# Performance work log

Hardware: AMD Instinct MI355X
Metric: run time of the kernel (lower is better)

Reference implementation:

```python
import jax, jax.numpy as jnp
import numpy as np

EPS = 1e-5
GROUPS = 8

def _bn(x, g, b, axes):
    # training-mode batch norm over `axes`, channel axis = 1
    m = jnp.mean(x, axis=axes, keepdims=True)
    v = jnp.var(x, axis=axes, keepdims=True)
    shp = (1, -1) + (1,) * (x.ndim - 2)
    return (x - m) / jnp.sqrt(v + EPS) * g.reshape(shp) + b.reshape(shp)

def setup_inputs() -> dict:
    key = jax.random.key(0)
    k0, k1, k2 = jax.random.split(key, 3)
    N, C, T, V = 64, 256, 64, 25
    out_planes = 256
    gp = out_planes // GROUPS  # 32
    x = jax.random.normal(k0, (N, C, T, V), jnp.float32)
    w_qkv = jax.random.normal(k1, (2 * out_planes, C), jnp.float32) * np.float32(np.sqrt(1.0 / C))
    relative = jax.random.normal(k2, (2 * gp, 2 * V - 1), jnp.float32) * np.float32(np.sqrt(1.0 / gp))
    return {
        "x": x,
        "w_qkv": w_qkv,
        "relative": relative,
        "bn_qkv_g": jnp.ones(2 * out_planes, jnp.float32),
        "bn_qkv_b": jnp.zeros(2 * out_planes, jnp.float32),
        "bn_sim_g": jnp.ones(3 * GROUPS, jnp.float32),
        "bn_sim_b": jnp.zeros(3 * GROUPS, jnp.float32),
        "bn_out_g": jnp.ones(2 * out_planes, jnp.float32),
        "bn_out_b": jnp.zeros(2 * out_planes, jnp.float32),
    }

def reference(x, w_qkv, relative, bn_qkv_g, bn_qkv_b, bn_sim_g, bn_sim_b, bn_out_g, bn_out_b):
    N, C, T, V = x.shape
    out_planes = w_qkv.shape[0] // 2
    gp = out_planes // GROUPS
    K = V  # kernel_size == V by construction
    # static relative index table
    qi = np.arange(K)[None, :]
    ki = np.arange(K)[:, None]
    flat_idx = (ki - qi + K - 1).reshape(-1)
    # mean over frames T (permute(0,2,1,3) then mean over dim1 == mean over axis 2)
    y = jnp.mean(x, axis=2)  # [N, C, V]
    # 1x1 conv qkv + BN1d
    qkv = _bn(jnp.einsum('oc,ncv->nov', w_qkv, y), bn_qkv_g, bn_qkv_b, (0, 2))
    qkv = qkv.reshape(N, GROUPS, 2 * gp, V)
    q, k, v = qkv[:, :, : gp // 2], qkv[:, :, gp // 2: gp], qkv[:, :, gp:]
    all_emb = relative[:, flat_idx].reshape(2 * gp, K, K)
    q_e, k_e, v_e = all_emb[: gp // 2], all_emb[gp // 2: gp], all_emb[gp:]
    qr = jnp.einsum('ngci,cij->ngij', q, q_e)
    kr = jnp.einsum('ngci,cij->ngij', k, k_e).swapaxes(2, 3)
    qk = jnp.einsum('ngci,ngcj->ngij', q, k)
    stacked = jnp.concatenate([qk, qr, kr], axis=1)  # [N, 3*groups, V, V]
    stacked = _bn(stacked, bn_sim_g, bn_sim_b, (0, 2, 3)).reshape(N, 3, GROUPS, V, V).sum(axis=1)
    sim = jax.nn.softmax(stacked, axis=3)  # [N, groups, V, V]
    sv = jnp.einsum('ngij,ngcj->ngci', sim, v)
    sve = jnp.einsum('ngij,cij->ngci', sim, v_e)
    so = jnp.concatenate([sv, sve], axis=-1).reshape(N, 2 * out_planes, V)
    o = _bn(so, bn_out_g, bn_out_b, (0, 2)).reshape(N, out_planes, 2, V).sum(axis=2)
    o = jax.nn.sigmoid(o)[:, :, None, :]  # [N, out_planes, 1, V]
    return x + x * o
```

## Files before the change

### kernel.cpp

```cpp
#include <hip/hip_runtime.h>
#include <cmath>

#define NN 64
#define CC 256
#define TT 64
#define VV 25
#define OO 512
#define GG 8
#define NV (NN*VV)
#define STK 625

__global__ __launch_bounds__(256) void k_mean(const float* __restrict__ x,
                                              float* __restrict__ y) {
    __shared__ float tile[TT * VV];
    int b = blockIdx.x;
    const float4* x4 = (const float4*)(x + (size_t)b * (TT * VV));
    float4* t4 = (float4*)tile;
    for (int i = threadIdx.x; i < (TT * VV) / 4; i += 256) t4[i] = x4[i];
    __syncthreads();
    if (threadIdx.x < VV) {
        float s = 0.f;
        #pragma unroll
        for (int t = 0; t < TT; ++t) s += tile[t * VV + threadIdx.x];
        y[(size_t)b * VV + threadIdx.x] = s * (1.0f / TT);
    }
}

__global__ __launch_bounds__(256) void k_gemm(const float* __restrict__ y,
                                              const float* __restrict__ w,
                                              float* __restrict__ qkv) {
    __shared__ float ys[CC][VV + 1];
    int n = blockIdx.x >> 3, oc = blockIdx.x & 7;
    const float* yp = y + (size_t)n * CC * VV;
    for (int i = threadIdx.x; i < CC * VV; i += 256) ys[i / VV][i % VV] = yp[i];
    __syncthreads();
    int t = threadIdx.x;
    if (t >= 200) return;
    int v = t % VV, o0 = t / VV;
    int obase = oc * 64 + o0;
    float acc[8] = {0, 0, 0, 0, 0, 0, 0, 0};
    for (int c = 0; c < CC; c += 4) {
        float y0 = ys[c][v], y1 = ys[c + 1][v], y2 = ys[c + 2][v], y3 = ys[c + 3][v];
        #pragma unroll
        for (int u = 0; u < 8; ++u) {
            const float4 w4 = *(const float4*)&w[(size_t)(obase + u * 8) * CC + c];
            acc[u] += y0 * w4.x + y1 * w4.y + y2 * w4.z + y3 * w4.w;
        }
    }
    #pragma unroll
    for (int u = 0; u < 8; ++u)
        qkv[((size_t)n * OO + obase + u * 8) * VV + v] = acc[u];
}

__global__ __launch_bounds__(256) void k_stats_nv(const float* __restrict__ t,
                                                  const float* __restrict__ g,
                                                  const float* __restrict__ b,
                                                  float* __restrict__ scale,
                                                  float* __restrict__ shift) {
    int ch = blockIdx.x;
    float s = 0.f, s2 = 0.f;
    for (int i = threadIdx.x; i < NV; i += 256) {
        int n = i / VV, v = i - n * VV;
        float val = t[((size_t)n * OO + ch) * VV + v];
        s += val; s2 += val * val;
    }
    __shared__ float ra[256], rb[256];
    ra[threadIdx.x] = s; rb[threadIdx.x] = s2;
    __syncthreads();
    for (int off = 128; off > 0; off >>= 1) {
        if (threadIdx.x < off) {
            ra[threadIdx.x] += ra[threadIdx.x + off];
            rb[threadIdx.x] += rb[threadIdx.x + off];
        }
        __syncthreads();
    }
    if (threadIdx.x == 0) {
        float m = ra[0] * (1.0f / NV);
        float var = rb[0] * (1.0f / NV) - m * m;
        float sc = g[ch] * rsqrtf(var + 1e-5f);
        scale[ch] = sc;
        shift[ch] = b[ch] - m * sc;
    }
}

__global__ __launch_bounds__(256) void k_scores(const float* __restrict__ qkv,
                                                const float* __restrict__ rel,
                                                const float* __restrict__ qsc,
                                                const float* __restrict__ qsh,
                                                float* __restrict__ stk) {
    int n = blockIdx.x >> 3, gidx = blockIdx.x & 7;
    __shared__ float qs[16][VV], ks[16][VV], rs[32][49];
    int t = threadIdx.x;
    for (int i = t; i < 32 * VV; i += 256) {
        int c = i / VV, v = i - c * VV;
        int o = gidx * 64 + c;
        float val = qkv[((size_t)n * OO + o) * VV + v] * qsc[o] + qsh[o];
        if (c < 16) qs[c][v] = val; else ks[c - 16][v] = val;
    }
    for (int i = t; i < 32 * 49; i += 256) rs[i / 49][i % 49] = rel[i];
    __syncthreads();
    for (int ij = t; ij < STK; ij += 256) {
        int i = ij / VV, j = ij - (ij / VV) * VV;
        float aqk = 0.f, aqr = 0.f, akr = 0.f;
        #pragma unroll
        for (int c = 0; c < 16; ++c) {
            float qv = qs[c][i], kv = ks[c][j];
            aqk += qv * kv;
            aqr += qv * rs[c][i - j + 24];
            akr += kv * rs[16 + c][j - i + 24];
        }
        size_t base = (size_t)n * 24;
        stk[(base + gidx) * STK + ij]      = aqk;
        stk[(base + 8 + gidx) * STK + ij]  = aqr;
        stk[(base + 16 + gidx) * STK + ij] = akr;
    }
}

__global__ __launch_bounds__(256) void k_stats24_a(const float* __restrict__ stk,
                                                   float* __restrict__ part) {
    int ch = blockIdx.x >> 4, chunk = blockIdx.x & 15;
    float s = 0.f, s2 = 0.f;
    for (int i = threadIdx.x; i < 4 * STK; i += 256) {
        int n = chunk * 4 + i / STK, r = i - (i / STK) * STK;
        float v = stk[((size_t)n * 24 + ch) * STK + r];
        s += v; s2 += v * v;
    }
    __shared__ float ra[256], rb[256];
    ra[threadIdx.x] = s; rb[threadIdx.x] = s2;
    __syncthreads();
    for (int off = 128; off > 0; off >>= 1) {
        if (threadIdx.x < off) {
            ra[threadIdx.x] += ra[threadIdx.x + off];
            rb[threadIdx.x] += rb[threadIdx.x + off];
        }
        __syncthreads();
    }
    if (threadIdx.x == 0) {
        part[(ch * 16 + chunk) * 2]     = ra[0];
        part[(ch * 16 + chunk) * 2 + 1] = rb[0];
    }
}

__global__ __launch_bounds__(64) void k_stats24_b(const float* __restrict__ part,
                                                  const float* __restrict__ g,
                                                  const float* __restrict__ b,
                                                  float* __restrict__ scale,
                                                  float* __restrict__ shift) {
    int ch = threadIdx.x;
    if (ch < 24) {
        float s = 0.f, s2 = 0.f;
        for (int k = 0; k < 16; ++k) {
            s  += part[(ch * 16 + k) * 2];
            s2 += part[(ch * 16 + k) * 2 + 1];
        }
        float m = s * (1.0f / 40000.0f);
        float var = s2 * (1.0f / 40000.0f) - m * m;
        float sc = g[ch] * rsqrtf(var + 1e-5f);
        scale[ch] = sc;
        shift[ch] = b[ch] - m * sc;
    }
}

__global__ __launch_bounds__(256) void k_attnout(const float* __restrict__ stk,
                                                 const float* __restrict__ qkv,
                                                 const float* __restrict__ rel,
                                                 const float* __restrict__ qsc,
                                                 const float* __restrict__ qsh,
                                                 const float* __restrict__ ssc,
                                                 const float* __restrict__ ssh,
                                                 float* __restrict__ so) {
    int n = blockIdx.x >> 3, gidx = blockIdx.x & 7;
    __shared__ float S[STK];
    __shared__ float vs[32][VV];
    __shared__ float rs[32][49];
    int t = threadIdx.x;
    const size_t sb = (size_t)n * 24 * STK;
    float sc0 = ssc[gidx],      sh0 = ssh[gidx];
    float sc1 = ssc[8 + gidx],  sh1 = ssh[8 + gidx];
    float sc2 = ssc[16 + gidx], sh2 = ssh[16 + gidx];
    for (int ij = t; ij < STK; ij += 256) {
        float a = stk[sb + (size_t)gidx * STK + ij] * sc0 + sh0;
        a += stk[sb + (size_t)(8 + gidx) * STK + ij] * sc1 + sh1;
        a += stk[sb + (size_t)(16 + gidx) * STK + ij] * sc2 + sh2;
        S[ij] = a;
    }
    for (int i = t; i < 32 * VV; i += 256) {
        int c = i / VV, v = i - (i / VV) * VV;
        int o = gidx * 64 + 32 + c;
        vs[c][v] = qkv[((size_t)n * OO + o) * VV + v] * qsc[o] + qsh[o];
    }
    for (int i = t; i < 32 * 49; i += 256) rs[i / 49][i % 49] = rel[32 * 49 + i];
    __syncthreads();
    if (t < VV) {
        int i = t;
        float m = -1e30f;
        #pragma unroll
        for (int j = 0; j < VV; ++j) m = fmaxf(m, S[i * VV + j]);
        float sum = 0.f;
        float e[VV];
        #pragma unroll
        for (int j = 0; j < VV; ++j) { e[j] = expf(S[i * VV + j] - m); sum += e[j]; }
        float inv = 1.0f / sum;
        #pragma unroll
        for (int j = 0; j < VV; ++j) S[i * VV + j] = e[j] * inv;
    }
    __syncthreads();
    for (int idx = t; idx < 32 * VV; idx += 256) {
        int c = idx / VV, i = idx - (idx / VV) * VV;
        float sv = 0.f, sve = 0.f;
        #pragma unroll
        for (int j = 0; j < VV; ++j) {
            float p = S[i * VV + j];
            sv  += p * vs[c][j];
            sve += p * rs[c][i - j + 24];
        }
        size_t o = (size_t)(gidx * 32 + c) * 2;
        so[((size_t)n * OO + o) * VV + i]     = sv;
        so[((size_t)n * OO + o + 1) * VV + i] = sve;
    }
}

__global__ __launch_bounds__(256) void k_final(const float* __restrict__ x,
                                               const float* __restrict__ so,
                                               const float* __restrict__ osc,
                                               const float* __restrict__ osh,
                                               float* __restrict__ out) {
    int b = blockIdx.x;
    int n = b >> 8, p = b & 255;
    __shared__ float orow[VV];
    if (threadIdx.x < VV) {
        int v = threadIdx.x;
        int o0 = 2 * p, o1 = 2 * p + 1;
        float a  = so[((size_t)n * OO + o0) * VV + v] * osc[o0] + osh[o0];
        float c2 = so[((size_t)n * OO + o1) * VV + v] * osc[o1] + osh[o1];
        float z = a + c2;
        orow[v] = 1.0f + 1.0f / (1.0f + expf(-z));
    }
    __syncthreads();
    const float4* x4 = (const float4*)(x + (size_t)b * (TT * VV));
    float4* y4 = (float4*)(out + (size_t)b * (TT * VV));
    for (int wv = threadIdx.x; wv < (TT * VV) / 4; wv += 256) {
        float4 xv = x4[wv];
        int e = 4 * wv;
        int v0 = e % VV;
        float4 r;
        int v;
        v = v0;                      r.x = xv.x * orow[v];
        v = v0 + 1; if (v >= VV) v -= VV; r.y = xv.y * orow[v];
        v = v0 + 2; if (v >= VV) v -= VV; r.z = xv.z * orow[v];
        v = v0 + 3; if (v >= VV) v -= VV; r.w = xv.w * orow[v];
        y4[wv] = r;
    }
}

extern "C" void kernel_launch(void* const* d_in, const int* in_sizes, int n_in,
                              void* d_out, int out_size, void* d_ws, size_t ws_size,
                              hipStream_t stream) {
    (void)in_sizes; (void)n_in; (void)out_size; (void)ws_size;
    const float* x        = (const float*)d_in[0];
    const float* w_qkv    = (const float*)d_in[1];
    const float* relative = (const float*)d_in[2];
    const float* bn_qkv_g = (const float*)d_in[3];
    const float* bn_qkv_b = (const float*)d_in[4];
    const float* bn_sim_g = (const float*)d_in[5];
    const float* bn_sim_b = (const float*)d_in[6];
    const float* bn_out_g = (const float*)d_in[7];
    const float* bn_out_b = (const float*)d_in[8];
    float* out = (float*)d_out;

    float* ws = (float*)d_ws;
    float* w_y    = ws;
    float* w_qkvp = ws + 409600;
    float* w_stk  = ws + 1228800;
    float* w_so   = ws + 2188800;
    float* qsc    = ws + 3008000;
    float* qsh    = qsc + 512;
    float* ssc    = qsh + 512;
    float* ssh    = ssc + 24;
    float* osc    = ssh + 24;
    float* osh    = osc + 512;
    float* w_part = osh + 512;

    k_mean<<<NN * CC, 256, 0, stream>>>(x, w_y);
    k_gemm<<<NN * 8, 256, 0, stream>>>(w_y, w_qkv, w_qkvp);
    k_stats_nv<<<OO, 256, 0, stream>>>(w_qkvp, bn_qkv_g, bn_qkv_b, qsc, qsh);
    k_scores<<<NN * GG, 256, 0, stream>>>(w_qkvp, relative, qsc, qsh, w_stk);
    k_stats24_a<<<24 * 16, 256, 0, stream>>>(w_stk, w_part);
    k_stats24_b<<<1, 64, 0, stream>>>(w_part, bn_sim_g, bn_sim_b, ssc, ssh);
    k_attnout<<<NN * GG, 256, 0, stream>>>(w_stk, w_qkvp, relative, qsc, qsh, ssc, ssh, w_so);
    k_stats_nv<<<OO, 256, 0, stream>>>(w_so, bn_out_g, bn_out_b, osc, osh);
    k_final<<<NN * CC, 256, 0, stream>>>(x, w_so, osc, osh, out);
}
```

Before: 281.4 us.

## Fuse middle stages into one cooperative kernel with grid syncs and atomic BN stats

New measurement: 364.2 us. 29.4% more time.

```diff
diff --git a/kernel.cpp b/kernel.cpp
--- a/kernel.cpp
+++ b/kernel.cpp
@@ -1,4 +1,5 @@
 #include <hip/hip_runtime.h>
+#include <hip/hip_cooperative_groups.h>
 #include <cmath>
 
 #define NN 64
@@ -10,10 +11,16 @@
 #define NV (NN*VV)
 #define STK 625
 
+namespace cg = cooperative_groups;
+
 __global__ __launch_bounds__(256) void k_mean(const float* __restrict__ x,
-                                              float* __restrict__ y) {
+                                              float* __restrict__ y,
+                                              float* __restrict__ accz) {
     __shared__ float tile[TT * VV];
     int b = blockIdx.x;
+    if (b == 0) {
+        for (int i = threadIdx.x; i < 2096; i += 256) accz[i] = 0.f;
+    }
     const float4* x4 = (const float4*)(x + (size_t)b * (TT * VV));
     float4* t4 = (float4*)tile;
     for (int i = threadIdx.x; i < (TT * VV) / 4; i += 256) t4[i] = x4[i];
@@ -26,213 +33,202 @@
     }
 }
 
-__global__ __launch_bounds__(256) void k_gemm(const float* __restrict__ y,
-                                              const float* __restrict__ w,
-                                              float* __restrict__ qkv) {
-    __shared__ float ys[CC][VV + 1];
-    int n = blockIdx.x >> 3, oc = blockIdx.x & 7;
-    const float* yp = y + (size_t)n * CC * VV;
-    for (int i = threadIdx.x; i < CC * VV; i += 256) ys[i / VV][i % VV] = yp[i];
-    __syncthreads();
-    int t = threadIdx.x;
-    if (t >= 200) return;
-    int v = t % VV, o0 = t / VV;
-    int obase = oc * 64 + o0;
-    float acc[8] = {0, 0, 0, 0, 0, 0, 0, 0};
-    for (int c = 0; c < CC; c += 4) {
-        float y0 = ys[c][v], y1 = ys[c + 1][v], y2 = ys[c + 2][v], y3 = ys[c + 3][v];
+__global__ __launch_bounds__(256, 2) void k_mid(const float* __restrict__ y,
+                                                const float* __restrict__ w,
+                                                const float* __restrict__ rel,
+                                                const float* __restrict__ gq,
+                                                const float* __restrict__ bq,
+                                                const float* __restrict__ gs,
+                                                const float* __restrict__ bs,
+                                                float* __restrict__ qacc,
+                                                float* __restrict__ sacc,
+                                                float* __restrict__ oacc,
+                                                float* __restrict__ so) {
+    cg::grid_group grid = cg::this_grid();
+
+    __shared__ __align__(16) float ys[CC * (VV + 1)];
+    __shared__ float qs[64 * (VV + 1)];
+    __shared__ float S3[3 * STK];
+    __shared__ float P[STK];
+    __shared__ float rs[32 * 49];
+    __shared__ float csc[64], csh[64];
+    __shared__ float simp[6];
+    __shared__ float sred[24];
+
+    const int tid = threadIdx.x;
+    const int nb = blockIdx.x >> 3, gb = blockIdx.x & 7;
+
+    {
+        const float* yp = y + (size_t)nb * (CC * VV);
+        for (int i = tid; i < CC * VV; i += 256) {
+            int c = i / VV, v = i - c * VV;
+            ys[c * (VV + 1) + v] = yp[i];
+        }
+        __syncthreads();
+        if (tid < 200) {
+            int v = tid % VV, o0 = tid / VV;
+            const float* wp = w + (size_t)(gb * 64 + o0) * CC;
+            float acc[8] = {0, 0, 0, 0, 0, 0, 0, 0};
+            for (int c = 0; c < CC; c += 4) {
+                float y0 = ys[c * (VV + 1) + v],       y1 = ys[(c + 1) * (VV + 1) + v];
+                float y2 = ys[(c + 2) * (VV + 1) + v], y3 = ys[(c + 3) * (VV + 1) + v];
+                #pragma unroll
+                for (int u = 0; u < 8; ++u) {
+                    const float4 w4 = *(const float4*)(wp + (size_t)u * 8 * CC + c);
+                    acc[u] += y0 * w4.x + y1 * w4.y + y2 * w4.z + y3 * w4.w;
+                }
+            }
+            #pragma unroll
+            for (int u = 0; u < 8; ++u) qs[(o0 + u * 8) * (VV + 1) + v] = acc[u];
+        }
+        __syncthreads();
+        if (tid < 64) {
+            float s = 0.f, s2 = 0.f;
+            #pragma unroll
+            for (int v = 0; v < VV; ++v) {
+                float val = qs[tid * (VV + 1) + v];
+                s += val; s2 += val * val;
+            }
+            atomicAdd(&qacc[gb * 64 + tid], s);
+            atomicAdd(&qacc[512 + gb * 64 + tid], s2);
+        }
+    }
+    grid.sync();
+
+    {
+        if (tid < 64) {
+            int ch = gb * 64 + tid;
+            float m = qacc[ch] * (1.0f / NV);
+            float var = qacc[512 + ch] * (1.0f / NV) - m * m;
+            float sc = gq[ch] * rsqrtf(var + 1e-5f);
+            csc[tid] = sc;
+            csh[tid] = bq[ch] - m * sc;
+        }
+        __syncthreads();
+        for (int i = tid; i < 64 * VV; i += 256) {
+            int c = i / VV, v = i - c * VV;
+            qs[c * (VV + 1) + v] = qs[c * (VV + 1) + v] * csc[c] + csh[c];
+        }
+        for (int i = tid; i < 32 * 49; i += 256) rs[i] = rel[i];
+        __syncthreads();
+        float ls0 = 0.f, ls1 = 0.f, ls2 = 0.f, ls3 = 0.f, ls4 = 0.f, ls5 = 0.f;
+        for (int ij = tid; ij < STK; ij += 256) {
+            int i = ij / VV, j = ij - (ij / VV) * VV;
+            float aqk = 0.f, aqr = 0.f, akr = 0.f;
+            #pragma unroll
+            for (int c = 0; c < 16; ++c) {
+                float qv = qs[c * (VV + 1) + i], kv = qs[(16 + c) * (VV + 1) + j];
+                aqk += qv * kv;
+                aqr += qv * rs[c * 49 + i - j + 24];
+                akr += kv * rs[(16 + c) * 49 + j - i + 24];
+            }
+            S3[ij] = aqk; S3[STK + ij] = aqr; S3[2 * STK + ij] = akr;
+            ls0 += aqk; ls1 += aqk * aqk;
+            ls2 += aqr; ls3 += aqr * aqr;
+            ls4 += akr; ls5 += akr * akr;
+        }
         #pragma unroll
-        for (int u = 0; u < 8; ++u) {
-            const float4 w4 = *(const float4*)&w[(size_t)(obase + u * 8) * CC + c];
-            acc[u] += y0 * w4.x + y1 * w4.y + y2 * w4.z + y3 * w4.w;
-        }
-    }
-    #pragma unroll
-    for (int u = 0; u < 8; ++u)
-        qkv[((size_t)n * OO + obase + u * 8) * VV + v] = acc[u];
-}
-
-__global__ __launch_bounds__(256) void k_stats_nv(const float* __restrict__ t,
-                                                  const float* __restrict__ g,
-                                                  const float* __restrict__ b,
-                                                  float* __restrict__ scale,
-                                                  float* __restrict__ shift) {
-    int ch = blockIdx.x;
-    float s = 0.f, s2 = 0.f;
-    for (int i = threadIdx.x; i < NV; i += 256) {
-        int n = i / VV, v = i - n * VV;
-        float val = t[((size_t)n * OO + ch) * VV + v];
-        s += val; s2 += val * val;
-    }
-    __shared__ float ra[256], rb[256];
-    ra[threadIdx.x] = s; rb[threadIdx.x] = s2;
-    __syncthreads();
-    for (int off = 128; off > 0; off >>= 1) {
-        if (threadIdx.x < off) {
-            ra[threadIdx.x] += ra[threadIdx.x + off];
-            rb[threadIdx.x] += rb[threadIdx.x + off];
-        }
-        __syncthreads();
-    }
-    if (threadIdx.x == 0) {
-        float m = ra[0] * (1.0f / NV);
-        float var = rb[0] * (1.0f / NV) - m * m;
-        float sc = g[ch] * rsqrtf(var + 1e-5f);
-        scale[ch] = sc;
-        shift[ch] = b[ch] - m * sc;
-    }
-}
-
-__global__ __launch_bounds__(256) void k_scores(const float* __restrict__ qkv,
-                                                const float* __restrict__ rel,
-                                                const float* __restrict__ qsc,
-                                                const float* __restrict__ qsh,
-                                                float* __restrict__ stk) {
-    int n = blockIdx.x >> 3, gidx = blockIdx.x & 7;
-    __shared__ float qs[16][VV], ks[16][VV], rs[32][49];
-    int t = threadIdx.x;
-    for (int i = t; i < 32 * VV; i += 256) {
-        int c = i / VV, v = i - c * VV;
-        int o = gidx * 64 + c;
-        float val = qkv[((size_t)n * OO + o) * VV + v] * qsc[o] + qsh[o];
-        if (c < 16) qs[c][v] = val; else ks[c - 16][v] = val;
-    }
-    for (int i = t; i < 32 * 49; i += 256) rs[i / 49][i % 49] = rel[i];
-    __syncthreads();
-    for (int ij = t; ij < STK; ij += 256) {
-        int i = ij / VV, j = ij - (ij / VV) * VV;
-        float aqk = 0.f, aqr = 0.f, akr = 0.f;
-        #pragma unroll
-        for (int c = 0; c < 16; ++c) {
-            float qv = qs[c][i], kv = ks[c][j];
-            aqk += qv * kv;
-            aqr += qv * rs[c][i - j + 24];
-            akr += kv * rs[16 + c][j - i + 24];
-        }
-        size_t base = (size_t)n * 24;
-        stk[(base + gidx) * STK + ij]      = aqk;
-        stk[(base + 8 + gidx) * STK + ij]  = aqr;
-        stk[(base + 16 + gidx) * STK + ij] = akr;
-    }
-}
-
-__global__ __launch_bounds__(256) void k_stats24_a(const float* __restrict__ stk,
-                                                   float* __restrict__ part) {
-    int ch = blockIdx.x >> 4, chunk = blockIdx.x & 15;
-    float s = 0.f, s2 = 0.f;
-    for (int i = threadIdx.x; i < 4 * STK; i += 256) {
-        int n = chunk * 4 + i / STK, r = i - (i / STK) * STK;
-        float v = stk[((size_t)n * 24 + ch) * STK + r];
-        s += v; s2 += v * v;
-    }
-    __shared__ float ra[256], rb[256];
-    ra[threadIdx.x] = s; rb[threadIdx.x] = s2;
-    __syncthreads();
-    for (int off = 128; off > 0; off >>= 1) {
-        if (threadIdx.x < off) {
-            ra[threadIdx.x] += ra[threadIdx.x + off];
-            rb[threadIdx.x] += rb[threadIdx.x + off];
-        }
-        __syncthreads();
-    }
-    if (threadIdx.x == 0) {
-        part[(ch * 16 + chunk) * 2]     = ra[0];
-        part[(ch * 16 + chunk) * 2 + 1] = rb[0];
-    }
-}
-
-__global__ __launch_bounds__(64) void k_stats24_b(const float* __restrict__ part,
-                                                  const float* __restrict__ g,
-                                                  const float* __restrict__ b,
-                                                  float* __restrict__ scale,
-                                                  float* __restrict__ shift) {
-    int ch = threadIdx.x;
-    if (ch < 24) {
-        float s = 0.f, s2 = 0.f;
-        for (int k = 0; k < 16; ++k) {
-            s  += part[(ch * 16 + k) * 2];
-            s2 += part[(ch * 16 + k) * 2 + 1];
-        }
-        float m = s * (1.0f / 40000.0f);
-        float var = s2 * (1.0f / 40000.0f) - m * m;
-        float sc = g[ch] * rsqrtf(var + 1e-5f);
-        scale[ch] = sc;
-        shift[ch] = b[ch] - m * sc;
-    }
-}
-
-__global__ __launch_bounds__(256) void k_attnout(const float* __restrict__ stk,
-                                                 const float* __restrict__ qkv,
-                                                 const float* __restrict__ rel,
-                                                 const float* __restrict__ qsc,
-                                                 const float* __restrict__ qsh,
-                                                 const float* __restrict__ ssc,
-                                                 const float* __restrict__ ssh,
-                                                 float* __restrict__ so) {
-    int n = blockIdx.x >> 3, gidx = blockIdx.x & 7;
-    __shared__ float S[STK];
-    __shared__ float vs[32][VV];
-    __shared__ float rs[32][49];
-    int t = threadIdx.x;
-    const size_t sb = (size_t)n * 24 * STK;
-    float sc0 = ssc[gidx],      sh0 = ssh[gidx];
-    float sc1 = ssc[8 + gidx],  sh1 = ssh[8 + gidx];
-    float sc2 = ssc[16 + gidx], sh2 = ssh[16 + gidx];
-    for (int ij = t; ij < STK; ij += 256) {
-        float a = stk[sb + (size_t)gidx * STK + ij] * sc0 + sh0;
-        a += stk[sb + (size_t)(8 + gidx) * STK + ij] * sc1 + sh1;
-        a += stk[sb + (size_t)(16 + gidx) * STK + ij] * sc2 + sh2;
-        S[ij] = a;
-    }
-    for (int i = t; i < 32 * VV; i += 256) {
-        int c = i / VV, v = i - (i / VV) * VV;
-        int o = gidx * 64 + 32 + c;
-        vs[c][v] = qkv[((size_t)n * OO + o) * VV + v] * qsc[o] + qsh[o];
-    }
-    for (int i = t; i < 32 * 49; i += 256) rs[i / 49][i % 49] = rel[32 * 49 + i];
-    __syncthreads();
-    if (t < VV) {
-        int i = t;
-        float m = -1e30f;
-        #pragma unroll
-        for (int j = 0; j < VV; ++j) m = fmaxf(m, S[i * VV + j]);
-        float sum = 0.f;
-        float e[VV];
-        #pragma unroll
-        for (int j = 0; j < VV; ++j) { e[j] = expf(S[i * VV + j] - m); sum += e[j]; }
-        float inv = 1.0f / sum;
-        #pragma unroll
-        for (int j = 0; j < VV; ++j) S[i * VV + j] = e[j] * inv;
-    }
-    __syncthreads();
-    for (int idx = t; idx < 32 * VV; idx += 256) {
-        int c = idx / VV, i = idx - (idx / VV) * VV;
-        float sv = 0.f, sve = 0.f;
-        #pragma unroll
-        for (int j = 0; j < VV; ++j) {
-            float p = S[i * VV + j];
-            sv  += p * vs[c][j];
-            sve += p * rs[c][i - j + 24];
-        }
-        size_t o = (size_t)(gidx * 32 + c) * 2;
-        so[((size_t)n * OO + o) * VV + i]     = sv;
-        so[((size_t)n * OO + o + 1) * VV + i] = sve;
+        for (int off = 32; off > 0; off >>= 1) {
+            ls0 += __shfl_down(ls0, off); ls1 += __shfl_down(ls1, off);
+            ls2 += __shfl_down(ls2, off); ls3 += __shfl_down(ls3, off);
+            ls4 += __shfl_down(ls4, off); ls5 += __shfl_down(ls5, off);
+        }
+        int lane = tid & 63, wid = tid >> 6;
+        if (lane == 0) {
+            sred[wid * 6 + 0] = ls0; sred[wid * 6 + 1] = ls1;
+            sred[wid * 6 + 2] = ls2; sred[wid * 6 + 3] = ls3;
+            sred[wid * 6 + 4] = ls4; sred[wid * 6 + 5] = ls5;
+        }
+        __syncthreads();
+        if (tid < 6) {
+            float t2 = sred[tid] + sred[6 + tid] + sred[12 + tid] + sred[18 + tid];
+            int ch = (tid >> 1) * 8 + gb;
+            atomicAdd(&sacc[(tid & 1) * 24 + ch], t2);
+        }
+    }
+    grid.sync();
+
+    {
+        if (tid < 3) {
+            int ch = tid * 8 + gb;
+            float m = sacc[ch] * (1.0f / 40000.0f);
+            float var = sacc[24 + ch] * (1.0f / 40000.0f) - m * m;
+            float sc = gs[ch] * rsqrtf(var + 1e-5f);
+            simp[tid * 2] = sc;
+            simp[tid * 2 + 1] = bs[ch] - m * sc;
+        }
+        __syncthreads();
+        for (int ij = tid; ij < STK; ij += 256)
+            P[ij] = S3[ij] * simp[0] + simp[1]
+                  + S3[STK + ij] * simp[2] + simp[3]
+                  + S3[2 * STK + ij] * simp[4] + simp[5];
+        for (int i = tid; i < 32 * 49; i += 256) rs[i] = rel[32 * 49 + i];
+        __syncthreads();
+        if (tid < VV) {
+            const int i = tid;
+            float mx = -1e30f;
+            #pragma unroll
+            for (int j = 0; j < VV; ++j) mx = fmaxf(mx, P[i * VV + j]);
+            float e[VV]; float sum = 0.f;
+            #pragma unroll
+            for (int j = 0; j < VV; ++j) { e[j] = expf(P[i * VV + j] - mx); sum += e[j]; }
+            float inv = 1.0f / sum;
+            #pragma unroll
+            for (int j = 0; j < VV; ++j) P[i * VV + j] = e[j] * inv;
+        }
+        __syncthreads();
+        float* svs  = ys;
+        float* sves = ys + 800;
+        for (int idx = tid; idx < 800; idx += 256) {
+            int c = idx / VV, i = idx - (idx / VV) * VV;
+            float sv = 0.f, sve = 0.f;
+            #pragma unroll
+            for (int j = 0; j < VV; ++j) {
+                float p = P[i * VV + j];
+                sv  += p * qs[(32 + c) * (VV + 1) + j];
+                sve += p * rs[c * 49 + i - j + 24];
+            }
+            svs[idx] = sv; sves[idx] = sve;
+        }
+        __syncthreads();
+        if (tid < 64) {
+            int c = tid >> 1;
+            const float* src = (tid & 1) ? (sves + c * VV) : (svs + c * VV);
+            float s = 0.f, s2 = 0.f;
+            #pragma unroll
+            for (int i = 0; i < VV; ++i) { float val = src[i]; s += val; s2 += val * val; }
+            atomicAdd(&oacc[gb * 64 + tid], s);
+            atomicAdd(&oacc[512 + gb * 64 + tid], s2);
+        }
+        float* sop = so + ((size_t)nb * OO + gb * 64) * VV;
+        for (int idx = tid; idx < 1600; idx += 256) {
+            int oc = idx / VV, i = idx - (idx / VV) * VV;
+            int c = oc >> 1;
+            sop[idx] = (oc & 1) ? sves[c * VV + i] : svs[c * VV + i];
+        }
     }
 }
 
 __global__ __launch_bounds__(256) void k_final(const float* __restrict__ x,
                                                const float* __restrict__ so,
-                                               const float* __restrict__ osc,
-                                               const float* __restrict__ osh,
+                                               const float* __restrict__ oacc,
+                                               const float* __restrict__ go,
+                                               const float* __restrict__ bo,
                                                float* __restrict__ out) {
     int b = blockIdx.x;
     int n = b >> 8, p = b & 255;
     __shared__ float orow[VV];
     if (threadIdx.x < VV) {
+        int o0 = 2 * p, o1 = 2 * p + 1;
+        float m0 = oacc[o0] * (1.0f / NV);
+        float var0 = oacc[512 + o0] * (1.0f / NV) - m0 * m0;
+        float sc0 = go[o0] * rsqrtf(var0 + 1e-5f), sh0 = bo[o0] - m0 * sc0;
+        float m1 = oacc[o1] * (1.0f / NV);
+        float var1 = oacc[512 + o1] * (1.0f / NV) - m1 * m1;
+        float sc1 = go[o1] * rsqrtf(var1 + 1e-5f), sh1 = bo[o1] - m1 * sc1;
         int v = threadIdx.x;
-        int o0 = 2 * p, o1 = 2 * p + 1;
-        float a  = so[((size_t)n * OO + o0) * VV + v] * osc[o0] + osh[o0];
-        float c2 = so[((size_t)n * OO + o1) * VV + v] * osc[o1] + osh[o1];
+        float a  = so[((size_t)n * OO + o0) * VV + v] * sc0 + sh0;
+        float c2 = so[((size_t)n * OO + o1) * VV + v] * sc1 + sh1;
         float z = a + c2;
         orow[v] = 1.0f + 1.0f / (1.0f + expf(-z));
     }
@@ -269,25 +265,19 @@
     float* out = (float*)d_out;
 
     float* ws = (float*)d_ws;
-    float* w_y    = ws;
-    float* w_qkvp = ws + 409600;
-    float* w_stk  = ws + 1228800;
-    float* w_so   = ws + 2188800;
-    float* qsc    = ws + 3008000;
-    float* qsh    = qsc + 512;
-    float* ssc    = qsh + 512;
-    float* ssh    = ssc + 24;
-    float* osc    = ssh + 24;
-    float* osh    = osc + 512;
-    float* w_part = osh + 512;
-
-    k_mean<<<NN * CC, 256, 0, stream>>>(x, w_y);
-    k_gemm<<<NN * 8, 256, 0, stream>>>(w_y, w_qkv, w_qkvp);
-    k_stats_nv<<<OO, 256, 0, stream>>>(w_qkvp, bn_qkv_g, bn_qkv_b, qsc, qsh);
-    k_scores<<<NN * GG, 256, 0, stream>>>(w_qkvp, relative, qsc, qsh, w_stk);
-    k_stats24_a<<<24 * 16, 256, 0, stream>>>(w_stk, w_part);
-    k_stats24_b<<<1, 64, 0, stream>>>(w_part, bn_sim_g, bn_sim_b, ssc, ssh);
-    k_attnout<<<NN * GG, 256, 0, stream>>>(w_stk, w_qkvp, relative, qsc, qsh, ssc, ssh, w_so);
-    k_stats_nv<<<OO, 256, 0, stream>>>(w_so, bn_out_g, bn_out_b, osc, osh);
-    k_final<<<NN * CC, 256, 0, stream>>>(x, w_so, osc, osh, out);
-}
+    float* w_y  = ws;
+    float* w_so = ws + 409600;
+    float* qacc = ws + 1228800;
+    float* sacc = qacc + 1024;
+    float* oacc = sacc + 48;
+
+    k_mean<<<NN * CC, 256, 0, stream>>>(x, w_y, qacc);
+
+    void* args[] = {(void*)&w_y, (void*)&w_qkv, (void*)&relative,
+                    (void*)&bn_qkv_g, (void*)&bn_qkv_b,
+                    (void*)&bn_sim_g, (void*)&bn_sim_b,
+                    (void*)&qacc, (void*)&sacc, (void*)&oacc, (void*)&w_so};
+    hipLaunchCooperativeKernel(k_mid, dim3(NN * GG), dim3(256), args, 0, stream);
+
+    k_final<<<NN * CC, 256, 0, stream>>>(x, w_so, oacc, bn_out_g, bn_out_b, out);
+}
```
